# Optimization experiments

Hardware: AMD Instinct MI355X
Metric: run time of the kernel (lower is better)

The kernel has to match this reference:

```python
import jax, jax.numpy as jnp
import numpy as np

N_Q_HEADS = 32
N_KV_HEADS = 8
GROUP = N_Q_HEADS // N_KV_HEADS  # 4


def _rope(x, cos, sin):
    # x: [b, s, h, d]; cos/sin: [s, d//2]. Complex rotation on (even, odd) pairs,
    # matching torch.view_as_complex on reshape(..., -1, 2).
    b, s, h, d = x.shape
    xr = x.reshape(b, s, h, d // 2, 2)
    x0, x1 = xr[..., 0], xr[..., 1]
    c = cos[None, :, None, :]
    sn = sin[None, :, None, :]
    o0 = x0 * c - x1 * sn
    o1 = x0 * sn + x1 * c
    return jnp.stack([o0, o1], axis=-1).reshape(b, s, h, d)


def setup_inputs() -> dict:
    key = jax.random.key(0)
    B, S, D = 2, 2048, 4096
    HD = D // N_Q_HEADS  # 128
    ks = jax.random.split(key, 8)
    x = jax.random.normal(ks[0], (B, S, D), jnp.float32)
    # True rotary table (theta = 10000), as cos/sin of shape [S, HD//2]
    inv_freq = 1.0 / (10000.0 ** (jnp.arange(0, HD, 2, dtype=jnp.float32) / HD))
    ang = jnp.outer(jnp.arange(S, dtype=jnp.float32), inv_freq)
    freqs_cos = jnp.cos(ang)
    freqs_sin = jnp.sin(ang)
    sc = 0.02
    qw = jax.random.normal(ks[1], (D, N_Q_HEADS * HD), jnp.float32) * sc
    qb = jax.random.normal(ks[2], (N_Q_HEADS * HD,), jnp.float32) * sc
    kw = jax.random.normal(ks[3], (D, N_KV_HEADS * HD), jnp.float32) * sc
    kb = jax.random.normal(ks[4], (N_KV_HEADS * HD,), jnp.float32) * sc
    vw = jax.random.normal(ks[5], (D, N_KV_HEADS * HD), jnp.float32) * sc
    vb = jax.random.normal(ks[6], (N_KV_HEADS * HD,), jnp.float32) * sc
    ow = jax.random.normal(ks[7], (D, D), jnp.float32) * sc
    return dict(x=x, freqs_cos=freqs_cos, freqs_sin=freqs_sin,
                qw=qw, qb=qb, kw=kw, kb=kb, vw=vw, vb=vb, ow=ow, start_pos=0)


def reference(x, freqs_cos, freqs_sin, qw, qb, kw, kb, vw, vb, ow, start_pos):
    b, s, dim = x.shape
    hd = dim // N_Q_HEADS
    q = (x @ qw + qb).reshape(b, s, N_Q_HEADS, hd)
    k = (x @ kw + kb).reshape(b, s, N_KV_HEADS, hd)
    v = (x @ vw + vb).reshape(b, s, N_KV_HEADS, hd)
    cos = freqs_cos[start_pos:start_pos + s]
    sin = freqs_sin[start_pos:start_pos + s]
    q = _rope(q, cos, sin)
    k = _rope(k, cos, sin)
    # start_pos == 0: cache write then slice is identity on fresh k/v.
    # GQA: query head h = kv_head * GROUP + g (matches torch repeat+reshape).
    q = q.transpose(0, 2, 1, 3).reshape(b, N_KV_HEADS, GROUP, s, hd)
    k = k.transpose(0, 2, 1, 3)  # [b, Hkv, s, hd]
    v = v.transpose(0, 2, 1, 3)
    scores = jnp.einsum('bhgqd,bhkd->bhgqk', q, k) / jnp.sqrt(jnp.float32(hd))
    causal = jnp.tril(jnp.ones((s, s), bool))
    scores = jnp.where(causal[None, None, None], scores, jnp.float32(-1e30))
    p = jax.nn.softmax(scores, axis=-1)
    o = jnp.einsum('bhgqk,bhkd->bhgqd', p, v)
    o = o.reshape(b, N_Q_HEADS, s, hd).transpose(0, 2, 1, 3).reshape(b, s, dim)
    return o @ ow
```

## Files before the change

kernel.cpp:

```cpp
#include <hip/hip_runtime.h>
#include <hip/hip_bf16.h>
#include <stdint.h>

typedef __bf16 bf16_t;
typedef __bf16 bf16x8 __attribute__((ext_vector_type(8)));
typedef __bf16 bf16x4 __attribute__((ext_vector_type(4)));
typedef float f32x4 __attribute__((ext_vector_type(4)));

typedef __attribute__((address_space(1))) unsigned gu32;
typedef __attribute__((address_space(3))) unsigned lu32;

__device__ __forceinline__ unsigned short f2bf(float f) {
  unsigned u = __builtin_bit_cast(unsigned, f);
  unsigned r = (u + 0x7FFFu + ((u >> 16) & 1u)) >> 16;
  return (unsigned short)r;
}

__device__ __forceinline__ void gload_lds16(const bf16_t* g, bf16_t* l) {
  __builtin_amdgcn_global_load_lds((const gu32*)(const void*)g, (lu32*)(void*)l, 16, 0, 0);
}

__global__ __launch_bounds__(256) void k_cvt_bf16(const float* __restrict__ in,
                                                  bf16_t* __restrict__ out, int n4) {
  int i = blockIdx.x * 256 + threadIdx.x;
  if (i >= n4) return;
  float4 v = ((const float4*)in)[i];
  ushort4 o;
  o.x = f2bf(v.x); o.y = f2bf(v.y); o.z = f2bf(v.z); o.w = f2bf(v.w);
  ((ushort4*)out)[i] = o;
}

__global__ __launch_bounds__(256) void k_transpose_cvt(const float* __restrict__ in,
                                                       bf16_t* __restrict__ out, int R, int C) {
  __shared__ float t[32][33];
  int c0 = blockIdx.x * 32, r0 = blockIdx.y * 32;
  int tx = threadIdx.x & 31, ty = threadIdx.x >> 5;
  #pragma unroll
  for (int r = 0; r < 4; ++r) {
    int rr = ty + r * 8;
    t[rr][tx] = in[(size_t)(r0 + rr) * C + c0 + tx];
  }
  __syncthreads();
  #pragma unroll
  for (int r = 0; r < 4; ++r) {
    int rr = ty + r * 8;
    ((unsigned short*)out)[(size_t)(c0 + rr) * R + r0 + tx] = f2bf(t[tx][rr]);
  }
}

__global__ __launch_bounds__(256) void k_transpose_bf16(const bf16_t* __restrict__ in,
                                                        bf16_t* __restrict__ out, int R, int C) {
  __shared__ unsigned short t[32][33];
  const unsigned short* ip = (const unsigned short*)in + (size_t)blockIdx.z * R * C;
  unsigned short* op = (unsigned short*)out + (size_t)blockIdx.z * R * C;
  int c0 = blockIdx.x * 32, r0 = blockIdx.y * 32;
  int tx = threadIdx.x & 31, ty = threadIdx.x >> 5;
  #pragma unroll
  for (int r = 0; r < 4; ++r) {
    int rr = ty + r * 8;
    t[rr][tx] = ip[(size_t)(r0 + rr) * C + c0 + tx];
  }
  __syncthreads();
  #pragma unroll
  for (int r = 0; r < 4; ++r) {
    int rr = ty + r * 8;
    op[(size_t)(c0 + rr) * R + r0 + tx] = t[tx][rr];
  }
}

#define BK 32
__global__ __launch_bounds__(256) void k_gemm_qkv(
    const bf16_t* __restrict__ A, const bf16_t* __restrict__ Bm,
    const float* __restrict__ qb, const float* __restrict__ kb, const float* __restrict__ vb,
    const float* __restrict__ cosT, const float* __restrict__ sinT,
    const int* __restrict__ start_pos,
    bf16_t* __restrict__ Qr, bf16_t* __restrict__ Kr, bf16_t* __restrict__ Vr) {
  __shared__ __attribute__((aligned(16))) bf16_t sA[128 * BK];
  __shared__ __attribute__((aligned(16))) bf16_t sB[128 * BK];
  const int tid = threadIdx.x;
  const int lane = tid & 63;
  const int wv = tid >> 6;
  const int wr = wv >> 1, wc = wv & 1;
  const int brow = blockIdx.x * 128;
  const int bcol = blockIdx.y * 128;
  const int K = 4096;
  const int l4 = lane >> 2;
  const int c8 = (lane & 3) * 8;
  const int fr = lane & 15;
  const int fq = lane >> 4;

  f32x4 acc[4][4];
  #pragma unroll
  for (int i = 0; i < 4; ++i)
    #pragma unroll
    for (int j = 0; j < 4; ++j) acc[i][j] = (f32x4){0.f, 0.f, 0.f, 0.f};

  for (int k0 = 0; k0 < K; k0 += BK) {
    #pragma unroll
    for (int r = 0; r < 2; ++r) {
      int chunk = r * 4 + wv;
      int row = chunk * 16 + l4;
      gload_lds16(A + (size_t)(brow + row) * K + k0 + c8, sA + chunk * 512);
      gload_lds16(Bm + (size_t)(bcol + row) * K + k0 + c8, sB + chunk * 512);
    }
    __syncthreads();
    bf16x8 af[4], bfv[4];
    #pragma unroll
    for (int mi = 0; mi < 4; ++mi)
      af[mi] = *(const bf16x8*)(sA + (wr * 64 + mi * 16 + fr) * BK + fq * 8);
    #pragma unroll
    for (int ni = 0; ni < 4; ++ni)
      bfv[ni] = *(const bf16x8*)(sB + (wc * 64 + ni * 16 + fr) * BK + fq * 8);
    #pragma unroll
    for (int mi = 0; mi < 4; ++mi)
      #pragma unroll
      for (int ni = 0; ni < 4; ++ni)
        acc[mi][ni] = __builtin_amdgcn_mfma_f32_16x16x32_bf16(af[mi], bfv[ni], acc[mi][ni], 0, 0, 0);
    __syncthreads();
  }

  const int sp = *start_pos;
  #pragma unroll
  for (int mi = 0; mi < 4; ++mi) {
    #pragma unroll
    for (int ni = 0; ni < 4; ++ni) {
      int col = bcol + wc * 64 + ni * 16 + fr;
      float bias = (col < 4096) ? qb[col] : (col < 5120 ? kb[col - 4096] : vb[col - 5120]);
      #pragma unroll
      for (int j = 0; j < 4; ++j) {
        int row = brow + wr * 64 + mi * 16 + fq * 4 + j;
        int b = row >> 11, s = row & 2047;
        int d = col & 127;
        float v = acc[mi][ni][j] + bias;
        float partner = __shfl_xor(v, 1);
        if (col < 5120) {
          int dd = d >> 1;
          float cc = cosT[(size_t)(sp + s) * 64 + dd];
          float sn = sinT[(size_t)(sp + s) * 64 + dd];
          v = (d & 1) ? (partner * sn + v * cc) : (v * cc - partner * sn);
        }
        unsigned short bvv = f2bf(v);
        if (col < 4096) {
          int h = col >> 7;
          ((unsigned short*)Qr)[(((size_t)b * 32 + h) * 2048 + s) * 128 + d] = bvv;
        } else if (col < 5120) {
          int hk = (col - 4096) >> 7;
          ((unsigned short*)Kr)[(((size_t)b * 8 + hk) * 2048 + s) * 128 + d] = bvv;
        } else {
          int hk = (col - 5120) >> 7;
          ((unsigned short*)Vr)[(((size_t)b * 8 + hk) * 2048 + s) * 128 + d] = bvv;
        }
      }
    }
  }
}

__global__ __launch_bounds__(256) void k_attn(
    const bf16_t* __restrict__ Qr, const bf16_t* __restrict__ Kr,
    const bf16_t* __restrict__ Vt, bf16_t* __restrict__ Ob) {
  __shared__ __attribute__((aligned(16))) bf16_t sK[2][4096];
  __shared__ __attribute__((aligned(16))) bf16_t sV[2][4096];
  __shared__ __attribute__((aligned(16))) bf16_t p_lds[4][2][16][40];

  const int tid = threadIdx.x;
  const int lane = tid & 63;
  const int w = tid >> 6;
  const int b = blockIdx.y >> 5, h = blockIdx.y & 31;
  const int hk = h >> 2;
  const int qt = (int)gridDim.x - 1 - (int)blockIdx.x;
  const int q0b = qt * 128;
  const int T = qt * 4 + 4;
  const bf16_t* Qb = Qr + (((size_t)b * 32 + h) * 2048) * 128;
  const bf16_t* Kb = Kr + (((size_t)b * 8 + hk) * 2048) * 128;
  const bf16_t* Vb = Vt + (((size_t)b * 8 + hk) * 128) * 2048;
  const int fr = lane & 15, fq = lane >> 4;
  const int qw0 = q0b + w * 32;
  const float sc = 0.08838834764831845f;

  const int c0 = w * 64 + lane;
  const int c1 = 256 + w * 64 + lane;
  const int krow0 = c0 >> 4, krow1 = c1 >> 4;
  const int ko0 = ((c0 & 15) << 4) ^ ((krow0 & 7) << 4);
  const int ko1 = ((c1 & 15) << 4) ^ ((krow1 & 7) << 4);
  const size_t ksrc0 = (size_t)krow0 * 128 + (ko0 >> 1);
  const size_t ksrc1 = (size_t)krow1 * 128 + (ko1 >> 1);
  const int vr0 = c0 >> 3, vr1 = c1 >> 3;
  const int vo0 = ((c0 & 7) << 4) ^ ((vr0 & 7) << 4);
  const int vo1 = ((c1 & 7) << 4) ^ ((vr1 & 7) << 4);
  const size_t vsrc0 = (size_t)(2 * vr0 + (vo0 >> 6)) * 2048 + ((vo0 & 63) >> 1);
  const size_t vsrc1 = (size_t)(2 * vr1 + (vo1 >> 6)) * 2048 + ((vo1 & 63) >> 1);
  const int ldsA = (w * 64) * 8;
  const int ldsB = (256 + w * 64) * 8;

  bf16x8 qf[2][4];
  #pragma unroll
  for (int f = 0; f < 2; ++f)
    #pragma unroll
    for (int c = 0; c < 4; ++c)
      qf[f][c] = *(const bf16x8*)(Qb + (size_t)(qw0 + f * 16 + fr) * 128 + c * 32 + fq * 8);

  f32x4 o[2][8];
  #pragma unroll
  for (int f = 0; f < 2; ++f)
    #pragma unroll
    for (int i = 0; i < 8; ++i) o[f][i] = (f32x4){0.f, 0.f, 0.f, 0.f};
  float m_s[2] = {-1e30f, -1e30f}, l_s[2] = {0.f, 0.f};

  const int kswz = (fr & 7) << 4;
  const int vlane = (fr >> 1) * 128 + ((((fr & 1) << 6) | (fq << 4)) ^ ((fr >> 1) << 4));

  auto STAGE = [&](int buf, int kv0) {
    const bf16_t* Kt = Kb + (size_t)kv0 * 128;
    const bf16_t* Vg = Vb + kv0;
    bf16_t* sk = &sK[buf][0];
    bf16_t* sv = &sV[buf][0];
    gload_lds16(Kt + ksrc0, sk + ldsA);
    gload_lds16(Kt + ksrc1, sk + ldsB);
    gload_lds16(Vg + vsrc0, sv + ldsA);
    gload_lds16(Vg + vsrc1, sv + ldsB);
  };

  STAGE(0, 0);
  int cur = 0;
  for (int t = 0; t < T; ++t) {
    const int kv0 = t * 32;
    if (t + 1 < T) {
      STAGE(cur ^ 1, kv0 + 32);
      asm volatile("s_waitcnt vmcnt(4)" ::: "memory");
    } else {
      asm volatile("s_waitcnt vmcnt(0)" ::: "memory");
    }
    __builtin_amdgcn_s_barrier();

    if (kv0 <= qw0 + 31) {
      const char* skc = (const char*)&sK[cur][0];
      const char* svc = (const char*)&sV[cur][0];
      f32x4 st[2][2];
      #pragma unroll
      for (int f = 0; f < 2; ++f)
        #pragma unroll
        for (int s2 = 0; s2 < 2; ++s2) st[f][s2] = (f32x4){0.f, 0.f, 0.f, 0.f};
      #pragma unroll
      for (int c = 0; c < 4; ++c) {
        const int off = (((c << 6) | (fq << 4)) ^ kswz);
        bf16x8 kf0 = *(const bf16x8*)(skc + fr * 256 + off);
        bf16x8 kf1 = *(const bf16x8*)(skc + 4096 + fr * 256 + off);
        st[0][0] = __builtin_amdgcn_mfma_f32_16x16x32_bf16(kf0, qf[0][c], st[0][0], 0, 0, 0);
        st[0][1] = __builtin_amdgcn_mfma_f32_16x16x32_bf16(kf1, qf[0][c], st[0][1], 0, 0, 0);
        st[1][0] = __builtin_amdgcn_mfma_f32_16x16x32_bf16(kf0, qf[1][c], st[1][0], 0, 0, 0);
        st[1][1] = __builtin_amdgcn_mfma_f32_16x16x32_bf16(kf1, qf[1][c], st[1][1], 0, 0, 0);
      }
      #pragma unroll
      for (int f = 0; f < 2; ++f) {
        const int qg = qw0 + f * 16 + fr;
        float p0[4], p1[4];
        float pm = -1e30f;
        #pragma unroll
        for (int j = 0; j < 4; ++j) {
          int kvr = kv0 + fq * 4 + j;
          float s0 = (kvr <= qg) ? st[f][0][j] * sc : -1e30f;
          float s1 = (kvr + 16 <= qg) ? st[f][1][j] * sc : -1e30f;
          p0[j] = s0; p1[j] = s1;
          pm = fmaxf(pm, fmaxf(s0, s1));
        }
        pm = fmaxf(pm, __shfl_xor(pm, 16));
        pm = fmaxf(pm, __shfl_xor(pm, 32));
        if (!__all(pm <= m_s[f] + 8.0f)) {
          float m_new = fmaxf(m_s[f], pm);
          float scf = __expf(m_s[f] - m_new);
          l_s[f] *= scf;
          #pragma unroll
          for (int j = 0; j < 4; ++j) {
            float sj = __shfl(scf, fq * 4 + j);
            #pragma unroll
            for (int df = 0; df < 8; ++df) o[f][df][j] *= sj;
          }
          m_s[f] = m_new;
        }
        float ps = 0.f;
        #pragma unroll
        for (int j = 0; j < 4; ++j) {
          p0[j] = __expf(p0[j] - m_s[f]);
          p1[j] = __expf(p1[j] - m_s[f]);
          ps += p0[j] + p1[j];
        }
        ps += __shfl_xor(ps, 16);
        ps += __shfl_xor(ps, 32);
        l_s[f] += ps;
        bf16x4 pk0, pk1;
        #pragma unroll
        for (int j = 0; j < 4; ++j) { pk0[j] = (bf16_t)p0[j]; pk1[j] = (bf16_t)p1[j]; }
        *(bf16x4*)&p_lds[w][f][fr][fq * 4] = pk0;
        *(bf16x4*)&p_lds[w][f][fr][16 + fq * 4] = pk1;
      }
      asm volatile("s_waitcnt lgkmcnt(0)" ::: "memory");
      bf16x8 pa0 = *(const bf16x8*)&p_lds[w][0][fr][fq * 8];
      bf16x8 pa1 = *(const bf16x8*)&p_lds[w][1][fr][fq * 8];
      #pragma unroll
      for (int df = 0; df < 8; ++df) {
        bf16x8 vf = *(const bf16x8*)(svc + df * 1024 + vlane);
        o[0][df] = __builtin_amdgcn_mfma_f32_16x16x32_bf16(pa0, vf, o[0][df], 0, 0, 0);
        o[1][df] = __builtin_amdgcn_mfma_f32_16x16x32_bf16(pa1, vf, o[1][df], 0, 0, 0);
      }
    }
    __builtin_amdgcn_sched_barrier(0);
    __builtin_amdgcn_s_barrier();
    cur ^= 1;
  }

  #pragma unroll
  for (int f = 0; f < 2; ++f) {
    #pragma unroll
    for (int j = 0; j < 4; ++j) {
      float lj = __shfl(l_s[f], fq * 4 + j);
      float rl = 1.f / lj;
      int srow = qw0 + f * 16 + fq * 4 + j;
      #pragma unroll
      for (int df = 0; df < 8; ++df) {
        int dcol = df * 16 + fr;
        ((unsigned short*)Ob)[((size_t)b * 2048 + srow) * 4096 + h * 128 + dcol] =
            f2bf(o[f][df][j] * rl);
      }
    }
  }
}

__global__ __launch_bounds__(256) void k_gemm_out(
    const bf16_t* __restrict__ A, const bf16_t* __restrict__ Bm, float* __restrict__ out) {
  __shared__ __attribute__((aligned(16))) bf16_t sA[128 * BK];
  __shared__ __attribute__((aligned(16))) bf16_t sB[128 * BK];
  const int tid = threadIdx.x;
  const int lane = tid & 63;
  const int wv = tid >> 6;
  const int wr = wv >> 1, wc = wv & 1;
  const int brow = blockIdx.x * 128;
  const int bcol = blockIdx.y * 128;
  const int K = 4096;
  const int l4 = lane >> 2;
  const int c8 = (lane & 3) * 8;
  const int fr = lane & 15;
  const int fq = lane >> 4;

  f32x4 acc[4][4];
  #pragma unroll
  for (int i = 0; i < 4; ++i)
    #pragma unroll
    for (int j = 0; j < 4; ++j) acc[i][j] = (f32x4){0.f, 0.f, 0.f, 0.f};

  for (int k0 = 0; k0 < K; k0 += BK) {
    #pragma unroll
    for (int r = 0; r < 2; ++r) {
      int chunk = r * 4 + wv;
      int row = chunk * 16 + l4;
      gload_lds16(A + (size_t)(brow + row) * K + k0 + c8, sA + chunk * 512);
      gload_lds16(Bm + (size_t)(bcol + row) * K + k0 + c8, sB + chunk * 512);
    }
    __syncthreads();
    bf16x8 af[4], bfv[4];
    #pragma unroll
    for (int mi = 0; mi < 4; ++mi)
      af[mi] = *(const bf16x8*)(sA + (wr * 64 + mi * 16 + fr) * BK + fq * 8);
    #pragma unroll
    for (int ni = 0; ni < 4; ++ni)
      bfv[ni] = *(const bf16x8*)(sB + (wc * 64 + ni * 16 + fr) * BK + fq * 8);
    #pragma unroll
    for (int mi = 0; mi < 4; ++mi)
      #pragma unroll
      for (int ni = 0; ni < 4; ++ni)
        acc[mi][ni] = __builtin_amdgcn_mfma_f32_16x16x32_bf16(af[mi], bfv[ni], acc[mi][ni], 0, 0, 0);
    __syncthreads();
  }

  #pragma unroll
  for (int mi = 0; mi < 4; ++mi)
    #pragma unroll
    for (int ni = 0; ni < 4; ++ni) {
      int col = bcol + wc * 64 + ni * 16 + fr;
      #pragma unroll
      for (int j = 0; j < 4; ++j) {
        int row = brow + wr * 64 + mi * 16 + fq * 4 + j;
        out[(size_t)row * 4096 + col] = acc[mi][ni][j];
      }
    }
}

extern "C" void kernel_launch(void* const* d_in, const int* in_sizes, int n_in,
                              void* d_out, int out_size, void* d_ws, size_t ws_size,
                              hipStream_t stream) {
  const float* x    = (const float*)d_in[0];
  const float* cosT = (const float*)d_in[1];
  const float* sinT = (const float*)d_in[2];
  const float* qw   = (const float*)d_in[3];
  const float* qb   = (const float*)d_in[4];
  const float* kw   = (const float*)d_in[5];
  const float* kb   = (const float*)d_in[6];
  const float* vw   = (const float*)d_in[7];
  const float* vb   = (const float*)d_in[8];
  const float* ow   = (const float*)d_in[9];
  const int*   sp   = (const int*)d_in[10];
  float* out = (float*)d_out;
  char* ws = (char*)d_ws;

  bf16_t* xb  = (bf16_t*)(ws + 0);
  bf16_t* Ob  = (bf16_t*)(ws + 0);
  bf16_t* wT  = (bf16_t*)(ws + (size_t)33554432);
  bf16_t* owT = (bf16_t*)(ws + (size_t)83886080);
  bf16_t* Qr  = (bf16_t*)(ws + (size_t)117440512);
  bf16_t* Kr  = (bf16_t*)(ws + (size_t)150994944);
  bf16_t* Vr  = (bf16_t*)(ws + (size_t)159383552);
  bf16_t* Vt  = (bf16_t*)(ws + (size_t)167772160);

  k_cvt_bf16<<<16384, 256, 0, stream>>>(x, xb, 2 * 2048 * 4096 / 4);
  k_transpose_cvt<<<dim3(128, 128), 256, 0, stream>>>(qw, wT, 4096, 4096);
  k_transpose_cvt<<<dim3(32, 128), 256, 0, stream>>>(kw, wT + (size_t)4096 * 4096, 4096, 1024);
  k_transpose_cvt<<<dim3(32, 128), 256, 0, stream>>>(vw, wT + (size_t)5120 * 4096, 4096, 1024);
  k_transpose_cvt<<<dim3(128, 128), 256, 0, stream>>>(ow, owT, 4096, 4096);

  k_gemm_qkv<<<dim3(32, 48), 256, 0, stream>>>(xb, wT, qb, kb, vb, cosT, sinT, sp, Qr, Kr, Vr);
  k_transpose_bf16<<<dim3(4, 64, 16), 256, 0, stream>>>(Vr, Vt, 2048, 128);
  k_attn<<<dim3(16, 64), 256, 0, stream>>>(Qr, Kr, Vt, Ob);
  k_gemm_out<<<dim3(32, 32), 256, 0, stream>>>(Ob, owT, out);
}
```

Baseline: 1.007 ms.

## Swizzle GEMM block order, stage QKV epilogue through LDS, add MFMA priority hints

Both GEMMs remap the linear block id so consecutive blocks (in groups of 8, matching the XCD count) work on neighbouring tiles, aiming for better L2 reuse of A and B. The QKV epilogue writes the bias/RoPE results into an LDS tile, then each thread emits 16-byte row-contiguous stores instead of scattered 2-byte ones, at the cost of extra shared memory and a barrier. The attention kernel wraps its MFMA loops in s_setprio and shrinks the P staging buffer to one slot per wave, reloading it per fragment with extra waits.

```diff
diff --git a/kernel.cpp b/kernel.cpp
--- a/kernel.cpp
+++ b/kernel.cpp
@@ -77,12 +77,15 @@
     bf16_t* __restrict__ Qr, bf16_t* __restrict__ Kr, bf16_t* __restrict__ Vr) {
   __shared__ __attribute__((aligned(16))) bf16_t sA[128 * BK];
   __shared__ __attribute__((aligned(16))) bf16_t sB[128 * BK];
+  __shared__ __attribute__((aligned(16))) bf16_t sET[128][132];
   const int tid = threadIdx.x;
   const int lane = tid & 63;
   const int wv = tid >> 6;
   const int wr = wv >> 1, wc = wv & 1;
-  const int brow = blockIdx.x * 128;
-  const int bcol = blockIdx.y * 128;
+  const int bid = blockIdx.y * gridDim.x + blockIdx.x;
+  const int swz = (bid & 7) * 192 + (bid >> 3);
+  const int brow = (swz & 31) * 128;
+  const int bcol = (swz >> 5) * 128;
   const int K = 4096;
   const int l4 = lane >> 2;
   const int c8 = (lane & 3) * 8;
@@ -120,38 +123,56 @@
   }
 
   const int sp = *start_pos;
+  const bool isQ = bcol < 4096;
+  const bool isV = bcol >= 5120;
+  const int s0 = brow & 2047;
   #pragma unroll
   for (int mi = 0; mi < 4; ++mi) {
     #pragma unroll
     for (int ni = 0; ni < 4; ++ni) {
-      int col = bcol + wc * 64 + ni * 16 + fr;
-      float bias = (col < 4096) ? qb[col] : (col < 5120 ? kb[col - 4096] : vb[col - 5120]);
+      int lc = wc * 64 + ni * 16 + fr;
+      float bias = isQ ? qb[bcol + lc] : (!isV ? kb[bcol - 4096 + lc] : vb[bcol - 5120 + lc]);
+      int lrb = wr * 64 + mi * 16 + fq * 4;
+      bf16x4 pk;
       #pragma unroll
       for (int j = 0; j < 4; ++j) {
-        int row = brow + wr * 64 + mi * 16 + fq * 4 + j;
-        int b = row >> 11, s = row & 2047;
-        int d = col & 127;
         float v = acc[mi][ni][j] + bias;
         float partner = __shfl_xor(v, 1);
-        if (col < 5120) {
-          int dd = d >> 1;
+        if (!isV) {
+          int dd = lc >> 1;
+          int s = s0 + lrb + j;
           float cc = cosT[(size_t)(sp + s) * 64 + dd];
           float sn = sinT[(size_t)(sp + s) * 64 + dd];
-          v = (d & 1) ? (partner * sn + v * cc) : (v * cc - partner * sn);
+          v = (lc & 1) ? (partner * sn + v * cc) : (v * cc - partner * sn);
         }
-        unsigned short bvv = f2bf(v);
-        if (col < 4096) {
-          int h = col >> 7;
-          ((unsigned short*)Qr)[(((size_t)b * 32 + h) * 2048 + s) * 128 + d] = bvv;
-        } else if (col < 5120) {
-          int hk = (col - 4096) >> 7;
-          ((unsigned short*)Kr)[(((size_t)b * 8 + hk) * 2048 + s) * 128 + d] = bvv;
-        } else {
-          int hk = (col - 5120) >> 7;
-          ((unsigned short*)Vr)[(((size_t)b * 8 + hk) * 2048 + s) * 128 + d] = bvv;
-        }
-      }
-    }
+        pk[j] = (bf16_t)v;
+      }
+      *(bf16x4*)&sET[lc][lrb] = pk;
+    }
+  }
+  __syncthreads();
+  const int b = brow >> 11;
+  unsigned short* dst;
+  if (isQ)
+    dst = (unsigned short*)Qr + (((size_t)b * 32 + (bcol >> 7)) * 2048 + s0) * 128;
+  else if (!isV)
+    dst = (unsigned short*)Kr + (((size_t)b * 8 + ((bcol - 4096) >> 7)) * 2048 + s0) * 128;
+  else
+    dst = (unsigned short*)Vr + (((size_t)b * 8 + ((bcol - 5120) >> 7)) * 2048 + s0) * 128;
+  #pragma unroll
+  for (int i = 0; i < 8; ++i) {
+    int chunk = i * 256 + tid;
+    int sl = chunk >> 4;
+    int dp = (chunk & 15) * 8;
+    unsigned short tmp[8];
+    #pragma unroll
+    for (int k = 0; k < 8; ++k) tmp[k] = ((unsigned short*)sET)[(dp + k) * 132 + sl];
+    uint4 ov;
+    ov.x = (unsigned)tmp[0] | ((unsigned)tmp[1] << 16);
+    ov.y = (unsigned)tmp[2] | ((unsigned)tmp[3] << 16);
+    ov.z = (unsigned)tmp[4] | ((unsigned)tmp[5] << 16);
+    ov.w = (unsigned)tmp[6] | ((unsigned)tmp[7] << 16);
+    *(uint4*)(dst + (size_t)sl * 128 + dp) = ov;
   }
 }
 
@@ -160,7 +181,7 @@
     const bf16_t* __restrict__ Vt, bf16_t* __restrict__ Ob) {
   __shared__ __attribute__((aligned(16))) bf16_t sK[2][4096];
   __shared__ __attribute__((aligned(16))) bf16_t sV[2][4096];
-  __shared__ __attribute__((aligned(16))) bf16_t p_lds[4][2][16][40];
+  __shared__ __attribute__((aligned(16))) bf16_t p_lds[4][16][40];
 
   const int tid = threadIdx.x;
   const int lane = tid & 63;
@@ -240,6 +261,7 @@
       for (int f = 0; f < 2; ++f)
         #pragma unroll
         for (int s2 = 0; s2 < 2; ++s2) st[f][s2] = (f32x4){0.f, 0.f, 0.f, 0.f};
+      __builtin_amdgcn_s_setprio(1);
       #pragma unroll
       for (int c = 0; c < 4; ++c) {
         const int off = (((c << 6) | (fq << 4)) ^ kswz);
@@ -250,6 +272,8 @@
         st[1][0] = __builtin_amdgcn_mfma_f32_16x16x32_bf16(kf0, qf[1][c], st[1][0], 0, 0, 0);
         st[1][1] = __builtin_amdgcn_mfma_f32_16x16x32_bf16(kf1, qf[1][c], st[1][1], 0, 0, 0);
       }
+      __builtin_amdgcn_s_setprio(0);
+      bf16x8 pa[2];
       #pragma unroll
       for (int f = 0; f < 2; ++f) {
         const int qg = qw0 + f * 16 + fr;
@@ -258,10 +282,10 @@
         #pragma unroll
         for (int j = 0; j < 4; ++j) {
           int kvr = kv0 + fq * 4 + j;
-          float s0 = (kvr <= qg) ? st[f][0][j] * sc : -1e30f;
-          float s1 = (kvr + 16 <= qg) ? st[f][1][j] * sc : -1e30f;
-          p0[j] = s0; p1[j] = s1;
-          pm = fmaxf(pm, fmaxf(s0, s1));
+          float s0v = (kvr <= qg) ? st[f][0][j] * sc : -1e30f;
+          float s1v = (kvr + 16 <= qg) ? st[f][1][j] * sc : -1e30f;
+          p0[j] = s0v; p1[j] = s1v;
+          pm = fmaxf(pm, fmaxf(s0v, s1v));
         }
         pm = fmaxf(pm, __shfl_xor(pm, 16));
         pm = fmaxf(pm, __shfl_xor(pm, 32));
@@ -290,18 +314,20 @@
         bf16x4 pk0, pk1;
         #pragma unroll
         for (int j = 0; j < 4; ++j) { pk0[j] = (bf16_t)p0[j]; pk1[j] = (bf16_t)p1[j]; }
-        *(bf16x4*)&p_lds[w][f][fr][fq * 4] = pk0;
-        *(bf16x4*)&p_lds[w][f][fr][16 + fq * 4] = pk1;
-      }
-      asm volatile("s_waitcnt lgkmcnt(0)" ::: "memory");
-      bf16x8 pa0 = *(const bf16x8*)&p_lds[w][0][fr][fq * 8];
-      bf16x8 pa1 = *(const bf16x8*)&p_lds[w][1][fr][fq * 8];
+        *(bf16x4*)&p_lds[w][fr][fq * 4] = pk0;
+        *(bf16x4*)&p_lds[w][fr][16 + fq * 4] = pk1;
+        asm volatile("s_waitcnt lgkmcnt(0)" ::: "memory");
+        pa[f] = *(const bf16x8*)&p_lds[w][fr][fq * 8];
+        asm volatile("s_waitcnt lgkmcnt(0)" ::: "memory");
+      }
+      __builtin_amdgcn_s_setprio(1);
       #pragma unroll
       for (int df = 0; df < 8; ++df) {
         bf16x8 vf = *(const bf16x8*)(svc + df * 1024 + vlane);
-        o[0][df] = __builtin_amdgcn_mfma_f32_16x16x32_bf16(pa0, vf, o[0][df], 0, 0, 0);
-        o[1][df] = __builtin_amdgcn_mfma_f32_16x16x32_bf16(pa1, vf, o[1][df], 0, 0, 0);
-      }
+        o[0][df] = __builtin_amdgcn_mfma_f32_16x16x32_bf16(pa[0], vf, o[0][df], 0, 0, 0);
+        o[1][df] = __builtin_amdgcn_mfma_f32_16x16x32_bf16(pa[1], vf, o[1][df], 0, 0, 0);
+      }
+      __builtin_amdgcn_s_setprio(0);
     }
     __builtin_amdgcn_sched_barrier(0);
     __builtin_amdgcn_s_barrier();
@@ -333,8 +359,10 @@
   const int lane = tid & 63;
   const int wv = tid >> 6;
   const int wr = wv >> 1, wc = wv & 1;
-  const int brow = blockIdx.x * 128;
-  const int bcol = blockIdx.y * 128;
+  const int bid = blockIdx.y * gridDim.x + blockIdx.x;
+  const int swz = (bid & 7) * 128 + (bid >> 3);
+  const int brow = (swz & 31) * 128;
+  const int bcol = (swz >> 5) * 128;
   const int K = 4096;
   const int l4 = lane >> 2;
   const int c8 = (lane & 3) * 8;
```

Measured after the change: 958.7 us. 4.8% less time.
